# Performance work log

Hardware: AMD Instinct MI355X
Metric: run time of the kernel (lower is better)

The kernel has to match this reference:

```python
import jax, jax.numpy as jnp
import numpy as np

B, T, N, D_OBJ = 8, 32, 10, 2048
N_VERB, N_OBJCLS = 157, 353
D_EMB, D_VERB = 512, 2048


def setup_inputs() -> dict:
    key = jax.random.key(0)
    k1, k2, k3, k4, k5 = jax.random.split(key, 5)
    objects_features = jax.random.normal(k1, (B, T, N, D_OBJ), dtype=jnp.float32)
    fm_context = jax.random.normal(k2, (B, T, D_VERB), dtype=jnp.float32)
    obj_id = jax.random.randint(k3, (B, T, N, N_OBJCLS), 0, 2, dtype=jnp.int32)
    W = jax.random.normal(k4, (D_OBJ, D_EMB), dtype=jnp.float32) * 0.02
    b = jnp.zeros((D_EMB,), dtype=jnp.float32)
    A_o2v = jnp.full((N_VERB, N_OBJCLS), 1.0 / N_VERB, dtype=jnp.float32)
    return {"objects_features": objects_features, "fm_context": fm_context,
            "obj_id": obj_id, "W": W, "b": b, "A_o2v": A_o2v}


def reference(objects_features, fm_context, obj_id, W, b, A_o2v):
    D = obj_id.shape[-1]
    # one-hot cleanup: all-zero row -> class 0; multi-hot row -> last nonzero class
    row_sum = obj_id.sum(-1)                                  # (B,T,N)
    last_nz = (D - 1) - jnp.argmax(jnp.flip(obj_id, -1), -1)  # last nonzero index
    cls = jnp.where(row_sum == 0, 0, last_nz)                 # (B,T,N)

    obj_embedded = objects_features @ W + b                   # (B,T,N,D_emb)

    # subA[b,t,n,v] = A_o2v[v, cls[b,t,n]]
    subA = A_o2v.T[cls]                                       # (B,T,N,V)

    afforded = jnp.einsum('btnv,btnd->btvd', subA, obj_embedded)  # (B,T,V,D_emb)

    V = A_o2v.shape[0]
    ctx = jnp.broadcast_to(fm_context[:, :, None, :],
                           (afforded.shape[0], afforded.shape[1], V, fm_context.shape[-1]))
    vo_actions = jnp.concatenate([afforded, ctx], axis=-1)    # (B,T,V,D_emb+D_verb)
    return vo_actions.mean(axis=1)                            # (B,V,D_emb+D_verb)
```

## Files before the change

### kernel.cpp

```cpp
#include <hip/hip_runtime.h>


typedef __attribute__((ext_vector_type(8))) short short8;
typedef __attribute__((ext_vector_type(4))) float f32x4;
typedef __attribute__((ext_vector_type(4))) unsigned short us4;

#define OFF_CLS  0
#define OFF_CNT  10240
#define OFF_CTX  16384
#define OFF_SAT  81920
#define OFF_FT   1064960
#define OFF_WT   11550720
#define OFF_G    13647872
#define OFF_PART 19939328

static __device__ inline unsigned short f2bf(float x) {
    unsigned int u = __builtin_bit_cast(unsigned int, x);
    u += 0x7fffu + ((u >> 16) & 1u);
    return (unsigned short)(u >> 16);
}

static __device__ inline void gl16(const void* g, void* l) {
    __builtin_amdgcn_global_load_lds(
        (__attribute__((address_space(1))) void*)(g),
        (__attribute__((address_space(3))) void*)(l), 16, 0, 0);
}

__global__ void k_cls(const int* __restrict__ obj_id, int* __restrict__ cls)
{
    int row  = blockIdx.x * 4 + (threadIdx.x >> 6);
    int lane = threadIdx.x & 63;
    if (row >= 2560) return;
    const int* p = obj_id + (size_t)row * 353;
    int last = -1;
    #pragma unroll
    for (int base = 0; base < 384; base += 64) {
        int idx = base + lane;
        int v = (idx < 353) ? p[idx] : 0;
        unsigned long long m = __ballot(v != 0);
        if (m) last = base + 63 - __clzll(m);
    }
    if (lane == 0) cls[row] = (last < 0) ? 0 : last;
}

__global__ void k_cvt_featT(const float* __restrict__ in, unsigned short* __restrict__ out)
{
    __shared__ float t[32][33];
    int bx = blockIdx.x;
    int b  = bx / 640;
    int r  = bx % 640;
    int it = r / 64, dt = r % 64;
    int tid = threadIdx.x;
    int rr = tid >> 3, cc = (tid & 7) * 4;
    float4 v = *(const float4*)&in[((size_t)b * 320 + it * 32 + rr) * 2048 + dt * 32 + cc];
    t[rr][cc] = v.x; t[rr][cc+1] = v.y; t[rr][cc+2] = v.z; t[rr][cc+3] = v.w;
    __syncthreads();
    us4 o = { f2bf(t[cc][rr]), f2bf(t[cc+1][rr]), f2bf(t[cc+2][rr]), f2bf(t[cc+3][rr]) };
    *(us4*)&out[((size_t)b * 2048 + dt * 32 + rr) * 320 + it * 32 + cc] = o;
}

__global__ void k_cvt_Wt(const float* __restrict__ W, unsigned short* __restrict__ Wt)
{
    __shared__ float t[32][33];
    int bx = blockIdx.x;
    int r0 = (bx >> 4) * 32, c0 = (bx & 15) * 32;
    int tid = threadIdx.x;
    int rr = tid >> 3, cc = (tid & 7) * 4;
    float4 v = *(const float4*)&W[(size_t)(r0 + rr) * 512 + c0 + cc];
    t[rr][cc] = v.x; t[rr][cc+1] = v.y; t[rr][cc+2] = v.z; t[rr][cc+3] = v.w;
    __syncthreads();
    us4 o = { f2bf(t[cc][rr]), f2bf(t[cc+1][rr]), f2bf(t[cc+2][rr]), f2bf(t[cc+3][rr]) };
    *(us4*)&Wt[(size_t)(c0 + rr) * 2048 + r0 + cc] = o;
}

__global__ void k_subAT(const float* __restrict__ A, const int* __restrict__ cls,
                        unsigned short* __restrict__ sAT)
{
    int id = blockIdx.x * 256 + threadIdx.x;
    int i = id % 320;
    int v = (id / 320) % 192;
    int b = id / (320 * 192);
    unsigned short o = 0;
    if (v < 157) o = f2bf(A[v * 353 + cls[b * 320 + i]] * (1.0f / 32.0f));
    sAT[id] = o;
}

__global__ void k_cnt(const float* __restrict__ A, const int* __restrict__ cls,
                      float* __restrict__ cnt)
{
    __shared__ int lc[320];
    int b = blockIdx.x, v = threadIdx.x;
    for (int i = v; i < 320; i += 192) lc[i] = cls[b * 320 + i];
    __syncthreads();
    float s = 0.f;
    if (v < 157) {
        for (int i = 0; i < 320; i++) s += A[v * 353 + lc[i]];
        s *= (1.0f / 32.0f);
    }
    cnt[b * 192 + v] = s;
}

template<int MODE>
__global__ __launch_bounds__(256) void k_gemm(
    const unsigned short* __restrict__ Ap, const unsigned short* __restrict__ Bp,
    void* __restrict__ Cp)
{
    constexpr int LDA = (MODE == 0) ? 320 : 2048;
    constexpr int LDB = (MODE == 0) ? 320 : 2048;
    constexpr int NT  = (MODE == 0) ? 10 : 16;

    int bx = blockIdx.x;
    int m0, n0, kb = 0;
    size_t aoff = 0, boff = 0, coff = 0;
    if (MODE == 0) {
        int b = bx / 48, r = bx % 48;
        m0 = (r >> 4) * 64; n0 = (r & 15) * 128;
        aoff = (size_t)b * 192 * 320; boff = (size_t)b * 2048 * 320;
        coff = (size_t)b * 192 * 2048;
    } else {
        int ks = bx & 3, r = bx >> 2;
        m0 = (r >> 2) * 64; n0 = (r & 3) * 128;
        kb = ks * 512; coff = (size_t)ks * 1536 * 512;
    }

    __shared__ __align__(16) unsigned short la[2][64 * 32];
    __shared__ __align__(16) unsigned short lb[2][128 * 32];

    int tid = threadIdx.x, lane = tid & 63, w = tid >> 6;
    int wm = (w >> 1) * 32, wn = (w & 1) * 64;
    int fr = lane & 15, fk = lane >> 4;

    int ra = tid >> 2;
    int kg = (tid & 3) ^ ((ra >> 1) & 3);
    const unsigned short* ga  = Ap + aoff + (size_t)(m0 + ra) * LDA + kg * 8 + kb;
    const unsigned short* gb0 = Bp + boff + (size_t)(n0 + ra) * LDB + kg * 8 + kb;
    const unsigned short* gb1 = gb0 + (size_t)64 * LDB;

    f32x4 acc[2][4] = {};

    auto stage = [&](int buf, int kk) {
        gl16(ga + kk,  &la[buf][tid * 8]);
        gl16(gb0 + kk, &lb[buf][tid * 8]);
        gl16(gb1 + kk, &lb[buf][(tid + 256) * 8]);
    };
    auto compute = [&](int buf) {
        short8 af[2], bf2[4];
        #pragma unroll
        for (int mi = 0; mi < 2; mi++) {
            int r = wm + mi * 16 + fr;
            int kgx = fk ^ ((r >> 1) & 3);
            af[mi] = *(const short8*)&la[buf][r * 32 + kgx * 8];
        }
        #pragma unroll
        for (int ni = 0; ni < 4; ni++) {
            int r = wn + ni * 16 + fr;
            int kgx = fk ^ ((r >> 1) & 3);
            bf2[ni] = *(const short8*)&lb[buf][r * 32 + kgx * 8];
        }
        #pragma unroll
        for (int mi = 0; mi < 2; mi++)
            #pragma unroll
            for (int ni = 0; ni < 4; ni++)
                acc[mi][ni] = __builtin_amdgcn_mfma_f32_16x16x32_bf16(
                    af[mi], bf2[ni], acc[mi][ni], 0, 0, 0);
    };

    stage(0, 0);
    __syncthreads();
    int cur = 0;
    #pragma unroll 1
    for (int t = 1; t < NT; t++) {
        stage(cur ^ 1, t * 32);
        compute(cur);
        __syncthreads();
        cur ^= 1;
    }
    compute(cur);

    if (MODE == 0) {
        unsigned short* Gp = (unsigned short*)Cp + coff;
        #pragma unroll
        for (int mi = 0; mi < 2; mi++) {
            int v0 = m0 + wm + mi * 16 + (fk << 2);
            #pragma unroll
            for (int ni = 0; ni < 4; ni++) {
                int d = n0 + wn + ni * 16 + fr;
                #pragma unroll
                for (int r = 0; r < 4; r++)
                    Gp[(size_t)(v0 + r) * 2048 + d] = f2bf(acc[mi][ni][r]);
            }
        }
    } else {
        float* P = (float*)Cp + coff;
        #pragma unroll
        for (int mi = 0; mi < 2; mi++) {
            int mrow = m0 + wm + mi * 16 + (fk << 2);
            #pragma unroll
            for (int ni = 0; ni < 4; ni++) {
                int e = n0 + wn + ni * 16 + fr;
                #pragma unroll
                for (int r = 0; r < 4; r++)
                    P[(size_t)(mrow + r) * 512 + e] = acc[mi][ni][r];
            }
        }
    }
}

__global__ void k_reduce(const float* __restrict__ part, const float* __restrict__ cnt,
                         const float* __restrict__ bias, float* __restrict__ out)
{
    int id = blockIdx.x * 256 + threadIdx.x;
    if (id >= 1536 * 128) return;
    int e4 = id & 127;
    int m  = id >> 7;
    int v = m % 192, b = m / 192;
    if (v >= 157) return;
    float4 s = ((const float4*)bias)[e4];
    float c = cnt[m];
    s.x *= c; s.y *= c; s.z *= c; s.w *= c;
    #pragma unroll
    for (int ks = 0; ks < 4; ks++) {
        float4 p = *(const float4*)&part[((size_t)ks * 1536 + m) * 512 + e4 * 4];
        s.x += p.x; s.y += p.y; s.z += p.z; s.w += p.w;
    }
    *(float4*)&out[((size_t)b * 157 + v) * 2560 + e4 * 4] = s;
}

__global__ void k_ctx_mean(const float* __restrict__ fm, float* __restrict__ ctx)
{
    int id = blockIdx.x * 256 + threadIdx.x;
    int b = id >> 11, d = id & 2047;
    const float* p = fm + (size_t)b * 32 * 2048 + d;
    float s = 0.f;
    #pragma unroll
    for (int t = 0; t < 32; t++) s += p[(size_t)t * 2048];
    ctx[id] = s * (1.0f / 32.0f);
}

__global__ void k_ctx_bcast(const float* __restrict__ ctx, float* __restrict__ out)
{
    int id = blockIdx.x * 256 + threadIdx.x;
    if (id >= 8 * 157 * 512) return;
    int q = id & 511;
    int bv = id >> 9;
    int b = bv / 157;
    float4 v = *(const float4*)&ctx[((size_t)b << 11) + q * 4];
    *(float4*)&out[(size_t)bv * 2560 + 512 + q * 4] = v;
}

extern "C" void kernel_launch(void* const* d_in, const int* in_sizes, int n_in,
                              void* d_out, int out_size, void* d_ws, size_t ws_size,
                              hipStream_t stream)
{
    const float* feat = (const float*)d_in[0];
    const float* fm   = (const float*)d_in[1];
    const int*   obj  = (const int*)d_in[2];
    const float* W    = (const float*)d_in[3];
    const float* bias = (const float*)d_in[4];
    const float* A    = (const float*)d_in[5];
    float* out = (float*)d_out;

    char* ws = (char*)d_ws;
    int*            cls   = (int*)(ws + OFF_CLS);
    float*          cnt   = (float*)(ws + OFF_CNT);
    float*          ctx   = (float*)(ws + OFF_CTX);
    unsigned short* sAT   = (unsigned short*)(ws + OFF_SAT);
    unsigned short* featT = (unsigned short*)(ws + OFF_FT);
    unsigned short* Wt    = (unsigned short*)(ws + OFF_WT);
    unsigned short* G     = (unsigned short*)(ws + OFF_G);
    float*          part  = (float*)(ws + OFF_PART);

    k_cls      <<<640, 256, 0, stream>>>(obj, cls);
    k_cvt_featT<<<5120, 256, 0, stream>>>(feat, featT);
    k_cvt_Wt   <<<1024, 256, 0, stream>>>(W, Wt);
    k_subAT    <<<1920, 256, 0, stream>>>(A, cls, sAT);
    k_cnt      <<<8, 192, 0, stream>>>(A, cls, cnt);
    k_gemm<0>  <<<384, 256, 0, stream>>>(sAT, featT, G);
    k_gemm<1>  <<<384, 256, 0, stream>>>(G, Wt, part);
    k_reduce   <<<768, 256, 0, stream>>>(part, cnt, bias, out);
    k_ctx_mean <<<64, 256, 0, stream>>>(fm, ctx);
    k_ctx_bcast<<<2512, 256, 0, stream>>>(ctx, out);
}
```

Baseline: 135.6 us.

## Reorder GEMMs to embed features first and fuse prep kernels into three launches

```diff
diff --git a/kernel.cpp b/kernel.cpp
--- a/kernel.cpp
+++ b/kernel.cpp
@@ -2,250 +2,286 @@
 
 
 typedef __attribute__((ext_vector_type(8))) short short8;
+typedef __attribute__((ext_vector_type(8))) unsigned short us8;
+typedef __attribute__((ext_vector_type(4))) unsigned short us4;
 typedef __attribute__((ext_vector_type(4))) float f32x4;
-typedef __attribute__((ext_vector_type(4))) unsigned short us4;
-
-#define OFF_CLS  0
-#define OFF_CNT  10240
-#define OFF_CTX  16384
-#define OFF_SAT  81920
-#define OFF_FT   1064960
-#define OFF_WT   11550720
-#define OFF_G    13647872
-#define OFF_PART 19939328
+
+#define OFF_CTX  0
+#define OFF_SAT  65536
+#define OFF_WT   1048576
+#define OFF_PART 3145728
 
 static __device__ inline unsigned short f2bf(float x) {
     unsigned int u = __builtin_bit_cast(unsigned int, x);
     u += 0x7fffu + ((u >> 16) & 1u);
     return (unsigned short)(u >> 16);
 }
-
 static __device__ inline void gl16(const void* g, void* l) {
     __builtin_amdgcn_global_load_lds(
         (__attribute__((address_space(1))) void*)(g),
         (__attribute__((address_space(3))) void*)(l), 16, 0, 0);
 }
 
-__global__ void k_cls(const int* __restrict__ obj_id, int* __restrict__ cls)
-{
-    int row  = blockIdx.x * 4 + (threadIdx.x >> 6);
-    int lane = threadIdx.x & 63;
-    if (row >= 2560) return;
-    const int* p = obj_id + (size_t)row * 353;
-    int last = -1;
-    #pragma unroll
-    for (int base = 0; base < 384; base += 64) {
-        int idx = base + lane;
-        int v = (idx < 353) ? p[idx] : 0;
-        unsigned long long m = __ballot(v != 0);
-        if (m) last = base + 63 - __clzll(m);
-    }
-    if (lane == 0) cls[row] = (last < 0) ? 0 : last;
-}
-
-__global__ void k_cvt_featT(const float* __restrict__ in, unsigned short* __restrict__ out)
+__global__ __launch_bounds__(256) void k_prep(
+    const float* __restrict__ W, const float* __restrict__ fm,
+    const int* __restrict__ obj, const float* __restrict__ A,
+    unsigned short* __restrict__ Wt, float* __restrict__ ctx,
+    unsigned short* __restrict__ sAT)
 {
     __shared__ float t[32][33];
+    __shared__ int lcls[64];
+    int bx = blockIdx.x, tid = threadIdx.x;
+
+    if (bx < 1024) {
+        int r0 = (bx >> 4) * 32, c0 = (bx & 15) * 32;
+        int rr = tid >> 3, cc = (tid & 7) * 4;
+        float4 v = *(const float4*)&W[(size_t)(r0 + rr) * 512 + c0 + cc];
+        t[rr][cc] = v.x; t[rr][cc+1] = v.y; t[rr][cc+2] = v.z; t[rr][cc+3] = v.w;
+        __syncthreads();
+        us4 o = { f2bf(t[cc][rr]), f2bf(t[cc+1][rr]), f2bf(t[cc+2][rr]), f2bf(t[cc+3][rr]) };
+        *(us4*)&Wt[(size_t)(c0 + rr) * 2048 + r0 + cc] = o;
+    } else if (bx < 1088) {
+        int id = (bx - 1024) * 256 + tid;
+        int b = id >> 11, d = id & 2047;
+        const float* p = fm + (size_t)b * 32 * 2048 + d;
+        float s = 0.f;
+        #pragma unroll
+        for (int tt = 0; tt < 32; tt++) s += p[(size_t)tt * 2048];
+        ctx[id] = s * (1.0f / 32.0f);
+    } else {
+        int blk = bx - 1088;
+        int b = blk / 5, i0 = (blk % 5) * 64;
+        int w = tid >> 6, lane = tid & 63;
+        for (int rr = 0; rr < 16; rr++) {
+            int il = w * 16 + rr;
+            const int* p = obj + ((size_t)b * 320 + i0 + il) * 353;
+            int last = -1;
+            #pragma unroll
+            for (int base = 0; base < 384; base += 64) {
+                int idx = base + lane;
+                int v = (idx < 353) ? p[idx] : 0;
+                unsigned long long m = __ballot(v != 0);
+                if (m) last = base + 63 - __clzll(m);
+            }
+            if (lane == 0) lcls[il] = (last < 0) ? 0 : last;
+        }
+        __syncthreads();
+        #pragma unroll
+        for (int q = 0; q < 6; q++) {
+            int u = q * 256 + tid;
+            int v = u >> 3, i8 = u & 7;
+            us8 o = {};
+            if (v < 157) {
+                #pragma unroll
+                for (int j = 0; j < 8; j++)
+                    o[j] = f2bf(A[v * 353 + lcls[i8 * 8 + j]] * (1.0f / 32.0f));
+            }
+            *(us8*)&sAT[((size_t)b * 192 + v) * 320 + i0 + i8 * 8] = o;
+        }
+    }
+}
+
+__global__ __launch_bounds__(256) void k_gemmE(
+    const float* __restrict__ feat, const unsigned short* __restrict__ Wt,
+    float* __restrict__ part)
+{
     int bx = blockIdx.x;
-    int b  = bx / 640;
-    int r  = bx % 640;
-    int it = r / 64, dt = r % 64;
-    int tid = threadIdx.x;
-    int rr = tid >> 3, cc = (tid & 7) * 4;
-    float4 v = *(const float4*)&in[((size_t)b * 320 + it * 32 + rr) * 2048 + dt * 32 + cc];
-    t[rr][cc] = v.x; t[rr][cc+1] = v.y; t[rr][cc+2] = v.z; t[rr][cc+3] = v.w;
-    __syncthreads();
-    us4 o = { f2bf(t[cc][rr]), f2bf(t[cc+1][rr]), f2bf(t[cc+2][rr]), f2bf(t[cc+3][rr]) };
-    *(us4*)&out[((size_t)b * 2048 + dt * 32 + rr) * 320 + it * 32 + cc] = o;
-}
-
-__global__ void k_cvt_Wt(const float* __restrict__ W, unsigned short* __restrict__ Wt)
-{
-    __shared__ float t[32][33];
-    int bx = blockIdx.x;
-    int r0 = (bx >> 4) * 32, c0 = (bx & 15) * 32;
-    int tid = threadIdx.x;
-    int rr = tid >> 3, cc = (tid & 7) * 4;
-    float4 v = *(const float4*)&W[(size_t)(r0 + rr) * 512 + c0 + cc];
-    t[rr][cc] = v.x; t[rr][cc+1] = v.y; t[rr][cc+2] = v.z; t[rr][cc+3] = v.w;
-    __syncthreads();
-    us4 o = { f2bf(t[cc][rr]), f2bf(t[cc+1][rr]), f2bf(t[cc+2][rr]), f2bf(t[cc+3][rr]) };
-    *(us4*)&Wt[(size_t)(c0 + rr) * 2048 + r0 + cc] = o;
-}
-
-__global__ void k_subAT(const float* __restrict__ A, const int* __restrict__ cls,
-                        unsigned short* __restrict__ sAT)
-{
-    int id = blockIdx.x * 256 + threadIdx.x;
-    int i = id % 320;
-    int v = (id / 320) % 192;
-    int b = id / (320 * 192);
-    unsigned short o = 0;
-    if (v < 157) o = f2bf(A[v * 353 + cls[b * 320 + i]] * (1.0f / 32.0f));
-    sAT[id] = o;
-}
-
-__global__ void k_cnt(const float* __restrict__ A, const int* __restrict__ cls,
-                      float* __restrict__ cnt)
-{
-    __shared__ int lc[320];
-    int b = blockIdx.x, v = threadIdx.x;
-    for (int i = v; i < 320; i += 192) lc[i] = cls[b * 320 + i];
-    __syncthreads();
-    float s = 0.f;
-    if (v < 157) {
-        for (int i = 0; i < 320; i++) s += A[v * 353 + lc[i]];
-        s *= (1.0f / 32.0f);
-    }
-    cnt[b * 192 + v] = s;
-}
-
-template<int MODE>
-__global__ __launch_bounds__(256) void k_gemm(
-    const unsigned short* __restrict__ Ap, const unsigned short* __restrict__ Bp,
-    void* __restrict__ Cp)
-{
-    constexpr int LDA = (MODE == 0) ? 320 : 2048;
-    constexpr int LDB = (MODE == 0) ? 320 : 2048;
-    constexpr int NT  = (MODE == 0) ? 10 : 16;
-
-    int bx = blockIdx.x;
-    int m0, n0, kb = 0;
-    size_t aoff = 0, boff = 0, coff = 0;
-    if (MODE == 0) {
-        int b = bx / 48, r = bx % 48;
-        m0 = (r >> 4) * 64; n0 = (r & 15) * 128;
-        aoff = (size_t)b * 192 * 320; boff = (size_t)b * 2048 * 320;
-        coff = (size_t)b * 192 * 2048;
-    } else {
-        int ks = bx & 3, r = bx >> 2;
-        m0 = (r >> 2) * 64; n0 = (r & 3) * 128;
-        kb = ks * 512; coff = (size_t)ks * 1536 * 512;
-    }
-
-    __shared__ __align__(16) unsigned short la[2][64 * 32];
-    __shared__ __align__(16) unsigned short lb[2][128 * 32];
+    int ks = bx & 3, nt = (bx >> 2) & 3, mt = bx >> 4;
+    int m0 = mt * 64, n0 = nt * 128, k0 = ks * 512;
+    int b = m0 / 320, i0 = m0 % 320;
+
+    __shared__ __align__(16) unsigned short la[2][64 * 64];
+    __shared__ __align__(16) unsigned short lb[2][128 * 64];
 
     int tid = threadIdx.x, lane = tid & 63, w = tid >> 6;
     int wm = (w >> 1) * 32, wn = (w & 1) * 64;
     int fr = lane & 15, fk = lane >> 4;
 
-    int ra = tid >> 2;
-    int kg = (tid & 3) ^ ((ra >> 1) & 3);
-    const unsigned short* ga  = Ap + aoff + (size_t)(m0 + ra) * LDA + kg * 8 + kb;
-    const unsigned short* gb0 = Bp + boff + (size_t)(n0 + ra) * LDB + kg * 8 + kb;
-    const unsigned short* gb1 = gb0 + (size_t)64 * LDB;
+    int ar = tid >> 2, acol = (tid & 3) * 16;
+    const float* gA = feat + (size_t)(m0 + ar) * 2048 + k0 + acol;
+    int asl0 = ((tid & 3) * 2 + 0) ^ (ar & 7);
+    int asl1 = ((tid & 3) * 2 + 1) ^ (ar & 7);
+
+    const unsigned short* gB[4];
+    #pragma unroll
+    for (int c = 0; c < 4; c++) {
+        int s = c * 256 + tid, er = s >> 3, ch = s & 7;
+        gB[c] = Wt + (size_t)(n0 + er) * 2048 + k0 + ((ch ^ (er & 7)) << 3);
+    }
 
     f32x4 acc[2][4] = {};
-
-    auto stage = [&](int buf, int kk) {
-        gl16(ga + kk,  &la[buf][tid * 8]);
-        gl16(gb0 + kk, &lb[buf][tid * 8]);
-        gl16(gb1 + kk, &lb[buf][(tid + 256) * 8]);
+    f32x4 a4[4];
+
+    auto loadA = [&](int kk) {
+        #pragma unroll
+        for (int j = 0; j < 4; j++) a4[j] = *(const f32x4*)(gA + kk + j * 4);
+    };
+    auto stageB = [&](int buf, int kk) {
+        #pragma unroll
+        for (int c = 0; c < 4; c++)
+            gl16(gB[c] + kk, &lb[buf][(c * 256 + tid) * 8]);
+    };
+    auto writeA = [&](int buf) {
+        us8 o0, o1;
+        #pragma unroll
+        for (int j = 0; j < 4; j++) { o0[j] = f2bf(a4[0][j]); o0[j+4] = f2bf(a4[1][j]); }
+        #pragma unroll
+        for (int j = 0; j < 4; j++) { o1[j] = f2bf(a4[2][j]); o1[j+4] = f2bf(a4[3][j]); }
+        *(us8*)&la[buf][ar * 64 + (asl0 << 3)] = o0;
+        *(us8*)&la[buf][ar * 64 + (asl1 << 3)] = o1;
     };
     auto compute = [&](int buf) {
-        short8 af[2], bf2[4];
-        #pragma unroll
-        for (int mi = 0; mi < 2; mi++) {
-            int r = wm + mi * 16 + fr;
-            int kgx = fk ^ ((r >> 1) & 3);
-            af[mi] = *(const short8*)&la[buf][r * 32 + kgx * 8];
-        }
-        #pragma unroll
-        for (int ni = 0; ni < 4; ni++) {
-            int r = wn + ni * 16 + fr;
-            int kgx = fk ^ ((r >> 1) & 3);
-            bf2[ni] = *(const short8*)&lb[buf][r * 32 + kgx * 8];
-        }
-        #pragma unroll
-        for (int mi = 0; mi < 2; mi++)
-            #pragma unroll
-            for (int ni = 0; ni < 4; ni++)
-                acc[mi][ni] = __builtin_amdgcn_mfma_f32_16x16x32_bf16(
-                    af[mi], bf2[ni], acc[mi][ni], 0, 0, 0);
-    };
-
-    stage(0, 0);
+        #pragma unroll
+        for (int k2 = 0; k2 < 2; k2++) {
+            short8 af[2], bf[4];
+            #pragma unroll
+            for (int mi = 0; mi < 2; mi++) {
+                int r = wm + mi * 16 + fr;
+                af[mi] = *(const short8*)&la[buf][r * 64 + (((k2 * 4 + fk) ^ (r & 7)) << 3)];
+            }
+            #pragma unroll
+            for (int ni = 0; ni < 4; ni++) {
+                int r = wn + ni * 16 + fr;
+                bf[ni] = *(const short8*)&lb[buf][r * 64 + (((k2 * 4 + fk) ^ (r & 7)) << 3)];
+            }
+            #pragma unroll
+            for (int mi = 0; mi < 2; mi++)
+                #pragma unroll
+                for (int ni = 0; ni < 4; ni++)
+                    acc[mi][ni] = __builtin_amdgcn_mfma_f32_16x16x32_bf16(
+                        af[mi], bf[ni], acc[mi][ni], 0, 0, 0);
+        }
+    };
+
+    loadA(0); stageB(0, 0); writeA(0);
     __syncthreads();
     int cur = 0;
     #pragma unroll 1
-    for (int t = 1; t < NT; t++) {
-        stage(cur ^ 1, t * 32);
+    for (int t = 0; t < 8; t++) {
+        if (t < 7) { loadA((t + 1) * 64); stageB(cur ^ 1, (t + 1) * 64); }
         compute(cur);
+        if (t < 7) writeA(cur ^ 1);
         __syncthreads();
         cur ^= 1;
     }
-    compute(cur);
-
-    if (MODE == 0) {
-        unsigned short* Gp = (unsigned short*)Cp + coff;
+
+    #pragma unroll
+    for (int mi = 0; mi < 2; mi++) {
+        int i = i0 + wm + mi * 16 + fk * 4;
+        #pragma unroll
+        for (int ni = 0; ni < 4; ni++) {
+            int e = n0 + wn + ni * 16 + fr;
+            *(f32x4*)&part[((size_t)(b * 512 + e) * 4 + ks) * 320 + i] = acc[mi][ni];
+        }
+    }
+}
+
+__global__ __launch_bounds__(256) void k_out(
+    const unsigned short* __restrict__ sAT, const float* __restrict__ part,
+    const float* __restrict__ bias, const float* __restrict__ ctx,
+    float* __restrict__ out)
+{
+    if (blockIdx.x >= 96) {
+        int id = (blockIdx.x - 96) * 256 + threadIdx.x;
+        int q = id & 511, bv = id >> 9, b = bv / 157;
+        float4 v = *(const float4*)&ctx[((size_t)b << 11) + q * 4];
+        *(float4*)&out[(size_t)bv * 2560 + 512 + q * 4] = v;
+        return;
+    }
+    int bx = blockIdx.x;
+    int b = bx / 12, r = bx % 12;
+    int v0 = (r >> 2) * 64, e0 = (r & 3) * 128;
+
+    __shared__ __align__(16) unsigned short la[2][64 * 32];
+    __shared__ __align__(16) unsigned short lb[2][128 * 32];
+
+    int tid = threadIdx.x, lane = tid & 63, w = tid >> 6;
+    int wm = (w >> 1) * 32, wn = (w & 1) * 64;
+    int fr = lane & 15, fk = lane >> 4;
+
+    int aer = tid >> 2, ach = tid & 3;
+    const unsigned short* gA = sAT + ((size_t)b * 192 + v0 + aer) * 320
+                                   + ((ach ^ (aer & 3)) << 3);
+    const float* pb = part + (size_t)b * 512 * 4 * 320;
+
+    f32x4 acc[2][4] = {};
+    f32x4 s0, s1, s2, s3;
+    float be0, be1, be2, be3;
+
+    auto loadB = [&](int kk) {
+        f32x4* sp[4] = { &s0, &s1, &s2, &s3 };
+        float* bp[4] = { &be0, &be1, &be2, &be3 };
+        #pragma unroll
+        for (int q = 0; q < 4; q++) {
+            int u = q * 256 + tid, e = u >> 3, i4 = u & 7;
+            const float* base = pb + (size_t)(e0 + e) * 4 * 320 + kk + i4 * 4;
+            f32x4 s = *(const f32x4*)(base);
+            s += *(const f32x4*)(base + 320);
+            s += *(const f32x4*)(base + 640);
+            s += *(const f32x4*)(base + 960);
+            *sp[q] = s;
+            *bp[q] = bias[e0 + e];
+        }
+    };
+    auto writeB = [&](int buf) {
+        f32x4 sv[4] = { s0, s1, s2, s3 };
+        float bv[4] = { be0, be1, be2, be3 };
+        #pragma unroll
+        for (int q = 0; q < 4; q++) {
+            int u = q * 256 + tid, e = u >> 3, i4 = u & 7;
+            f32x4 s = sv[q];
+            float be = bv[q];
+            us4 o = { f2bf(s[0] + be), f2bf(s[1] + be), f2bf(s[2] + be), f2bf(s[3] + be) };
+            *(us4*)&lb[buf][e * 32 + ((((i4 >> 1) ^ (e & 3)) << 3) + (i4 & 1) * 4)] = o;
+        }
+    };
+    auto compute = [&](int buf) {
+        short8 af[2], bf[4];
         #pragma unroll
         for (int mi = 0; mi < 2; mi++) {
-            int v0 = m0 + wm + mi * 16 + (fk << 2);
-            #pragma unroll
-            for (int ni = 0; ni < 4; ni++) {
-                int d = n0 + wn + ni * 16 + fr;
-                #pragma unroll
-                for (int r = 0; r < 4; r++)
-                    Gp[(size_t)(v0 + r) * 2048 + d] = f2bf(acc[mi][ni][r]);
-            }
-        }
-    } else {
-        float* P = (float*)Cp + coff;
-        #pragma unroll
-        for (int mi = 0; mi < 2; mi++) {
-            int mrow = m0 + wm + mi * 16 + (fk << 2);
-            #pragma unroll
-            for (int ni = 0; ni < 4; ni++) {
-                int e = n0 + wn + ni * 16 + fr;
-                #pragma unroll
-                for (int r = 0; r < 4; r++)
-                    P[(size_t)(mrow + r) * 512 + e] = acc[mi][ni][r];
-            }
-        }
-    }
-}
-
-__global__ void k_reduce(const float* __restrict__ part, const float* __restrict__ cnt,
-                         const float* __restrict__ bias, float* __restrict__ out)
-{
-    int id = blockIdx.x * 256 + threadIdx.x;
-    if (id >= 1536 * 128) return;
-    int e4 = id & 127;
-    int m  = id >> 7;
-    int v = m % 192, b = m / 192;
-    if (v >= 157) return;
-    float4 s = ((const float4*)bias)[e4];
-    float c = cnt[m];
-    s.x *= c; s.y *= c; s.z *= c; s.w *= c;
+            int rr = wm + mi * 16 + fr;
+            af[mi] = *(const short8*)&la[buf][rr * 32 + ((fk ^ (rr & 3)) << 3)];
+        }
+        #pragma unroll
+        for (int ni = 0; ni < 4; ni++) {
+            int rr = wn + ni * 16 + fr;
+            bf[ni] = *(const short8*)&lb[buf][rr * 32 + ((fk ^ (rr & 3)) << 3)];
+        }
+        #pragma unroll
+        for (int mi = 0; mi < 2; mi++)
+            #pragma unroll
+            for (int ni = 0; ni < 4; ni++)
+                acc[mi][ni] = __builtin_amdgcn_mfma_f32_16x16x32_bf16(
+                    af[mi], bf[ni], acc[mi][ni], 0, 0, 0);
+    };
+
+    gl16(gA, &la[0][tid * 8]);
+    loadB(0); writeB(0);
+    __syncthreads();
+    int cur = 0;
+    #pragma unroll 1
+    for (int t = 0; t < 10; t++) {
+        if (t < 9) { gl16(gA + (t + 1) * 32, &la[cur ^ 1][tid * 8]); loadB((t + 1) * 32); }
+        compute(cur);
+        if (t < 9) writeB(cur ^ 1);
+        __syncthreads();
+        cur ^= 1;
+    }
+
     #pragma unroll
-    for (int ks = 0; ks < 4; ks++) {
-        float4 p = *(const float4*)&part[((size_t)ks * 1536 + m) * 512 + e4 * 4];
-        s.x += p.x; s.y += p.y; s.z += p.z; s.w += p.w;
-    }
-    *(float4*)&out[((size_t)b * 157 + v) * 2560 + e4 * 4] = s;
-}
-
-__global__ void k_ctx_mean(const float* __restrict__ fm, float* __restrict__ ctx)
-{
-    int id = blockIdx.x * 256 + threadIdx.x;
-    int b = id >> 11, d = id & 2047;
-    const float* p = fm + (size_t)b * 32 * 2048 + d;
-    float s = 0.f;
-    #pragma unroll
-    for (int t = 0; t < 32; t++) s += p[(size_t)t * 2048];
-    ctx[id] = s * (1.0f / 32.0f);
-}
-
-__global__ void k_ctx_bcast(const float* __restrict__ ctx, float* __restrict__ out)
-{
-    int id = blockIdx.x * 256 + threadIdx.x;
-    if (id >= 8 * 157 * 512) return;
-    int q = id & 511;
-    int bv = id >> 9;
-    int b = bv / 157;
-    float4 v = *(const float4*)&ctx[((size_t)b << 11) + q * 4];
-    *(float4*)&out[(size_t)bv * 2560 + 512 + q * 4] = v;
+    for (int mi = 0; mi < 2; mi++) {
+        int vb = v0 + wm + mi * 16 + fk * 4;
+        #pragma unroll
+        for (int ni = 0; ni < 4; ni++) {
+            int e = e0 + wn + ni * 16 + fr;
+            #pragma unroll
+            for (int rr = 0; rr < 4; rr++) {
+                int v = vb + rr;
+                if (v < 157)
+                    out[((size_t)b * 157 + v) * 2560 + e] = acc[mi][ni][rr];
+            }
+        }
+    }
 }
 
 extern "C" void kernel_launch(void* const* d_in, const int* in_sizes, int n_in,
@@ -261,23 +297,12 @@
     float* out = (float*)d_out;
 
     char* ws = (char*)d_ws;
-    int*            cls   = (int*)(ws + OFF_CLS);
-    float*          cnt   = (float*)(ws + OFF_CNT);
-    float*          ctx   = (float*)(ws + OFF_CTX);
-    unsigned short* sAT   = (unsigned short*)(ws + OFF_SAT);
-    unsigned short* featT = (unsigned short*)(ws + OFF_FT);
-    unsigned short* Wt    = (unsigned short*)(ws + OFF_WT);
-    unsigned short* G     = (unsigned short*)(ws + OFF_G);
-    float*          part  = (float*)(ws + OFF_PART);
-
-    k_cls      <<<640, 256, 0, stream>>>(obj, cls);
-    k_cvt_featT<<<5120, 256, 0, stream>>>(feat, featT);
-    k_cvt_Wt   <<<1024, 256, 0, stream>>>(W, Wt);
-    k_subAT    <<<1920, 256, 0, stream>>>(A, cls, sAT);
-    k_cnt      <<<8, 192, 0, stream>>>(A, cls, cnt);
-    k_gemm<0>  <<<384, 256, 0, stream>>>(sAT, featT, G);
-    k_gemm<1>  <<<384, 256, 0, stream>>>(G, Wt, part);
-    k_reduce   <<<768, 256, 0, stream>>>(part, cnt, bias, out);
-    k_ctx_mean <<<64, 256, 0, stream>>>(fm, ctx);
-    k_ctx_bcast<<<2512, 256, 0, stream>>>(ctx, out);
-}
+    float*          ctx  = (float*)(ws + OFF_CTX);
+    unsigned short* sAT  = (unsigned short*)(ws + OFF_SAT);
+    unsigned short* Wt   = (unsigned short*)(ws + OFF_WT);
+    float*          part = (float*)(ws + OFF_PART);
+
+    k_prep <<<1128, 256, 0, stream>>>(W, fm, obj, A, Wt, ctx, sAT);
+    k_gemmE<<<640, 256, 0, stream>>>(feat, Wt, part);
+    k_out  <<<2608, 256, 0, stream>>>(sAT, part, bias, ctx, out);
+}
```

New measurement: 128.9 us. -4.9%, faster.
